# Optimization experiments

Hardware: AMD Instinct MI355X
Metric: run time of the kernel (lower is better)

## Reference

```python
import jax, jax.numpy as jnp
import numpy as np

SIGMA = 1.0
RADIUS = 4  # skimage.filters.gaussian: truncate=4.0 -> radius=int(4.0*1.0+0.5)=4 (9 taps)
NBINS = 256  # skimage.filters.threshold_otsu default


def _gauss_kernel(dtype):
    x = jnp.arange(-RADIUS, RADIUS + 1, dtype=dtype)
    k = jnp.exp(-0.5 * (x / SIGMA) ** 2)
    return k / k.sum()


def _blur(img):
    # img: [B, H, W]; separable Gaussian, 'nearest' (edge) boundary like scipy/skimage.
    k = _gauss_kernel(img.dtype)
    p = jnp.pad(img, ((0, 0), (RADIUS, RADIUS), (0, 0)), mode='edge')
    out = jax.lax.conv_general_dilated(p[:, None], k.reshape(1, 1, 2 * RADIUS + 1, 1),
                                       (1, 1), 'VALID')[:, 0]
    p = jnp.pad(out, ((0, 0), (0, 0), (RADIUS, RADIUS)), mode='edge')
    out = jax.lax.conv_general_dilated(p[:, None], k.reshape(1, 1, 1, 2 * RADIUS + 1),
                                       (1, 1), 'VALID')[:, 0]
    return out


def _otsu(img):
    # img: [H, W] -> scalar Otsu threshold (256-bin histogram over [min, max]).
    lo, hi = img.min(), img.max()
    width = (hi - lo) / NBINS
    idx = jnp.clip(jnp.floor((img - lo) / jnp.maximum(width, 1e-12)).astype(jnp.int32),
                   0, NBINS - 1)
    counts = jnp.zeros(NBINS, img.dtype).at[idx.ravel()].add(1.0)
    centers = lo + (jnp.arange(NBINS, dtype=img.dtype) + 0.5) * width
    w1 = jnp.cumsum(counts)                      # class-0 weight
    w2 = jnp.cumsum(counts[::-1])[::-1]          # class-1 weight
    cs = jnp.cumsum(counts * centers)
    rcs = jnp.cumsum((counts * centers)[::-1])[::-1]
    m1 = cs / jnp.maximum(w1, 1e-12)
    m2 = rcs / jnp.maximum(w2, 1e-12)
    var12 = w1[:-1] * w2[1:] * (m1[:-1] - m2[1:]) ** 2
    return centers[jnp.argmax(var12)]


def reference(x):
    # x: [B, 4, H, W]; channel 0 = thermal (normalized mean=std=0.5), last 3 = RGB.
    thermal = jnp.clip(x[:, 0] * 0.5 + 0.5, 0.0, 1.0)          # denormalize [B,H,W]
    blurred = _blur(thermal)
    t = jax.vmap(_otsu)(blurred)                               # [B]
    mask = jnp.where(blurred > t[:, None, None], 1.0, blurred)  # soft alpha mask
    rgb = x[:, -3:]                                            # [B,3,H,W]
    alpha = mask[:, None]                                      # [B,1,H,W]
    # skimage rgba2rgb with white background: clip(alpha*rgb + (1-alpha)*1)
    return jnp.clip(alpha * rgb + (1.0 - alpha), 0.0, 1.0)


def setup_inputs() -> dict:
    key = jax.random.key(0)
    x = jax.random.normal(key, (32, 4, 512, 512), dtype=jnp.float32)
    return {"x": x}
```

## Files before the change

### kernel.cpp

```cpp
#include <hip/hip_runtime.h>
#include <math.h>

#pragma clang fp contract(off)

struct GaussW { float w[9]; };

__global__ __launch_bounds__(256) void blur_kernel(const float* __restrict__ x,
                                                   float* __restrict__ blurred,
                                                   float* __restrict__ pmin,
                                                   float* __restrict__ pmax,
                                                   unsigned* __restrict__ hist, GaussW gw) {
    #pragma clang fp contract(off)
    __shared__ float s_in[72][72];
    __shared__ float s_vb[64][72];
    const int tid = threadIdx.x;
    const int b = blockIdx.z;
    const int r0 = blockIdx.y * 64, c0 = blockIdx.x * 64;
    if (blockIdx.x == 0 && blockIdx.y == 0) hist[b * 256 + tid] = 0u;
    const float* img0 = x + (size_t)b * 4 * 262144;

    for (int i = tid; i < 72 * 72; i += 256) {
        int r = i / 72, c = i - r * 72;
        int gr = min(max(r0 + r - 4, 0), 511);
        int gc = min(max(c0 + c - 4, 0), 511);
        float v = img0[gr * 512 + gc];
        s_in[r][c] = fminf(fmaxf(v * 0.5f + 0.5f, 0.0f), 1.0f);
    }
    __syncthreads();
    for (int i = tid; i < 1152; i += 256) {
        int sr = (i / 72) * 4, c = i % 72;
        float t0 = s_in[sr + 0][c], t1 = s_in[sr + 1][c], t2 = s_in[sr + 2][c];
        float t3 = s_in[sr + 3][c], t4 = s_in[sr + 4][c], t5 = s_in[sr + 5][c];
        float t6 = s_in[sr + 6][c], t7 = s_in[sr + 7][c], t8 = s_in[sr + 8][c];
        float t9 = s_in[sr + 9][c], t10 = s_in[sr + 10][c], t11 = s_in[sr + 11][c];
        {
            float q0 = t0 * gw.w[0], q1 = t1 * gw.w[1], q2 = t2 * gw.w[2], q3 = t3 * gw.w[3];
            float q4 = t4 * gw.w[4], q5 = t5 * gw.w[5], q6 = t6 * gw.w[6], q7 = t7 * gw.w[7];
            float acc = ((q0 + q1) + (q2 + q3)) + ((q4 + q5) + (q6 + q7));
            s_vb[sr + 0][c] = acc + t8 * gw.w[8];
        }
        {
            float q0 = t1 * gw.w[0], q1 = t2 * gw.w[1], q2 = t3 * gw.w[2], q3 = t4 * gw.w[3];
            float q4 = t5 * gw.w[4], q5 = t6 * gw.w[5], q6 = t7 * gw.w[6], q7 = t8 * gw.w[7];
            float acc = ((q0 + q1) + (q2 + q3)) + ((q4 + q5) + (q6 + q7));
            s_vb[sr + 1][c] = acc + t9 * gw.w[8];
        }
        {
            float q0 = t2 * gw.w[0], q1 = t3 * gw.w[1], q2 = t4 * gw.w[2], q3 = t5 * gw.w[3];
            float q4 = t6 * gw.w[4], q5 = t7 * gw.w[5], q6 = t8 * gw.w[6], q7 = t9 * gw.w[7];
            float acc = ((q0 + q1) + (q2 + q3)) + ((q4 + q5) + (q6 + q7));
            s_vb[sr + 2][c] = acc + t10 * gw.w[8];
        }
        {
            float q0 = t3 * gw.w[0], q1 = t4 * gw.w[1], q2 = t5 * gw.w[2], q3 = t6 * gw.w[3];
            float q4 = t7 * gw.w[4], q5 = t8 * gw.w[5], q6 = t9 * gw.w[6], q7 = t10 * gw.w[7];
            float acc = ((q0 + q1) + (q2 + q3)) + ((q4 + q5) + (q6 + q7));
            s_vb[sr + 3][c] = acc + t11 * gw.w[8];
        }
    }
    __syncthreads();
    float lmin = 1e30f, lmax = -1e30f;
    float* bimg = blurred + (size_t)b * 262144;
    for (int i = tid; i < 1024; i += 256) {
        int r = i >> 4, cc = (i & 15) * 4;
        float4 va = *(const float4*)&s_vb[r][cc];
        float4 vb = *(const float4*)&s_vb[r][cc + 4];
        float4 vc = *(const float4*)&s_vb[r][cc + 8];
        float t0 = va.x, t1 = va.y, t2 = va.z, t3 = va.w;
        float t4 = vb.x, t5 = vb.y, t6 = vb.z, t7 = vb.w;
        float t8 = vc.x, t9 = vc.y, t10 = vc.z, t11 = vc.w;
        float4 o;
        {
            float q0 = t0 * gw.w[0], q1 = t1 * gw.w[1], q2 = t2 * gw.w[2], q3 = t3 * gw.w[3];
            float q4 = t4 * gw.w[4], q5 = t5 * gw.w[5], q6 = t6 * gw.w[6], q7 = t7 * gw.w[7];
            float acc = ((q0 + q1) + (q2 + q3)) + ((q4 + q5) + (q6 + q7));
            o.x = acc + t8 * gw.w[8];
        }
        {
            float q0 = t1 * gw.w[0], q1 = t2 * gw.w[1], q2 = t3 * gw.w[2], q3 = t4 * gw.w[3];
            float q4 = t5 * gw.w[4], q5 = t6 * gw.w[5], q6 = t7 * gw.w[6], q7 = t8 * gw.w[7];
            float acc = ((q0 + q1) + (q2 + q3)) + ((q4 + q5) + (q6 + q7));
            o.y = acc + t9 * gw.w[8];
        }
        {
            float q0 = t2 * gw.w[0], q1 = t3 * gw.w[1], q2 = t4 * gw.w[2], q3 = t5 * gw.w[3];
            float q4 = t6 * gw.w[4], q5 = t7 * gw.w[5], q6 = t8 * gw.w[6], q7 = t9 * gw.w[7];
            float acc = ((q0 + q1) + (q2 + q3)) + ((q4 + q5) + (q6 + q7));
            o.z = acc + t10 * gw.w[8];
        }
        {
            float q0 = t3 * gw.w[0], q1 = t4 * gw.w[1], q2 = t5 * gw.w[2], q3 = t6 * gw.w[3];
            float q4 = t7 * gw.w[4], q5 = t8 * gw.w[5], q6 = t9 * gw.w[6], q7 = t10 * gw.w[7];
            float acc = ((q0 + q1) + (q2 + q3)) + ((q4 + q5) + (q6 + q7));
            o.w = acc + t11 * gw.w[8];
        }
        *(float4*)&bimg[(size_t)(r0 + r) * 512 + (c0 + cc)] = o;
        lmin = fminf(fminf(fminf(lmin, o.x), fminf(o.y, o.z)), o.w);
        lmax = fmaxf(fmaxf(fmaxf(lmax, o.x), fmaxf(o.y, o.z)), o.w);
    }
    for (int off = 32; off >= 1; off >>= 1) {
        lmin = fminf(lmin, __shfl_down(lmin, off));
        lmax = fmaxf(lmax, __shfl_down(lmax, off));
    }
    __shared__ float smin[4], smax[4];
    int wave = tid >> 6, lane = tid & 63;
    if (lane == 0) { smin[wave] = lmin; smax[wave] = lmax; }
    __syncthreads();
    if (tid == 0) {
        float mn = fminf(fminf(smin[0], smin[1]), fminf(smin[2], smin[3]));
        float mx = fmaxf(fmaxf(smax[0], smax[1]), fmaxf(smax[2], smax[3]));
        int bid = blockIdx.y * 8 + blockIdx.x;
        pmin[b * 64 + bid] = mn;
        pmax[b * 64 + bid] = mx;
    }
}

__global__ __launch_bounds__(256) void hist_kernel(const float* __restrict__ blurred,
                                                   const float* __restrict__ pmin,
                                                   const float* __restrict__ pmax,
                                                   unsigned* __restrict__ hist) {
    #pragma clang fp contract(off)
    const int b = blockIdx.y;
    __shared__ unsigned sh[2048];
    __shared__ float s_lo, s_hi;
    for (int i = threadIdx.x; i < 2048; i += 256) sh[i] = 0u;
    int wv = threadIdx.x >> 6, ln = threadIdx.x & 63;
    if (wv == 0) {
        float v = pmin[b * 64 + ln];
        for (int off = 32; off >= 1; off >>= 1) v = fminf(v, __shfl_down(v, off));
        if (ln == 0) s_lo = v;
    } else if (wv == 1) {
        float v = pmax[b * 64 + ln];
        for (int off = 32; off >= 1; off >>= 1) v = fmaxf(v, __shfl_down(v, off));
        if (ln == 0) s_hi = v;
    }
    __syncthreads();
    const float lo = s_lo, hi = s_hi;
    const float width = (hi - lo) * 0.00390625f;
    const float denom = fmaxf(width, 1e-12f);
    const int copy = threadIdx.x & 7;
    const float4* img = (const float4*)(blurred + (size_t)b * 262144);
    for (int i = blockIdx.x * 256 + threadIdx.x; i < 65536; i += gridDim.x * 256) {
        float4 v = img[i];
        int i0 = min(max((int)floorf((v.x - lo) / denom), 0), 255);
        int i1 = min(max((int)floorf((v.y - lo) / denom), 0), 255);
        int i2 = min(max((int)floorf((v.z - lo) / denom), 0), 255);
        int i3 = min(max((int)floorf((v.w - lo) / denom), 0), 255);
        atomicAdd(&sh[i0 * 8 + copy], 1u);
        atomicAdd(&sh[i1 * 8 + copy], 1u);
        atomicAdd(&sh[i2 * 8 + copy], 1u);
        atomicAdd(&sh[i3 * 8 + copy], 1u);
    }
    __syncthreads();
    unsigned cnt = 0;
    int base = threadIdx.x * 8;
#pragma unroll
    for (int k = 0; k < 8; ++k) cnt += sh[base + k];
    if (cnt) atomicAdd(&hist[b * 256 + threadIdx.x], cnt);
}

__global__ __launch_bounds__(256) void otsu_kernel(const unsigned* __restrict__ hist,
                                                   const float* __restrict__ pmin,
                                                   const float* __restrict__ pmax,
                                                   float* __restrict__ t) {
    #pragma clang fp contract(off)
    __shared__ float counts[256], centers[256], w1[256], w2[256], cs[256], rcs[256];
    __shared__ float s_lo, s_hi;
    const int b = blockIdx.x, tid = threadIdx.x;
    const int wv = tid >> 6, ln = tid & 63;
    if (wv == 0) {
        float v = pmin[b * 64 + ln];
        for (int off = 32; off >= 1; off >>= 1) v = fminf(v, __shfl_down(v, off));
        if (ln == 0) s_lo = v;
    } else if (wv == 1) {
        float v = pmax[b * 64 + ln];
        for (int off = 32; off >= 1; off >>= 1) v = fmaxf(v, __shfl_down(v, off));
        if (ln == 0) s_hi = v;
    }
    __syncthreads();
    const float lo = s_lo, hi = s_hi;
    const float width = (hi - lo) * 0.00390625f;
    counts[tid] = (float)hist[b * 256 + tid];
    centers[tid] = lo + ((float)tid + 0.5f) * width;
    __syncthreads();
    if (ln == 0) {
        if (wv == 0) {
            float a = 0.f;
            for (int i0 = 0; i0 < 256; i0 += 8) {
                float c0 = counts[i0+0], c1 = counts[i0+1], c2 = counts[i0+2], c3 = counts[i0+3];
                float c4 = counts[i0+4], c5 = counts[i0+5], c6 = counts[i0+6], c7 = counts[i0+7];
                a = a + c0; w1[i0+0] = a; a = a + c1; w1[i0+1] = a;
                a = a + c2; w1[i0+2] = a; a = a + c3; w1[i0+3] = a;
                a = a + c4; w1[i0+4] = a; a = a + c5; w1[i0+5] = a;
                a = a + c6; w1[i0+6] = a; a = a + c7; w1[i0+7] = a;
            }
        } else if (wv == 1) {
            float a = 0.f;
            for (int i0 = 255; i0 >= 7; i0 -= 8) {
                float c0 = counts[i0-0], c1 = counts[i0-1], c2 = counts[i0-2], c3 = counts[i0-3];
                float c4 = counts[i0-4], c5 = counts[i0-5], c6 = counts[i0-6], c7 = counts[i0-7];
                a = a + c0; w2[i0-0] = a; a = a + c1; w2[i0-1] = a;
                a = a + c2; w2[i0-2] = a; a = a + c3; w2[i0-3] = a;
                a = a + c4; w2[i0-4] = a; a = a + c5; w2[i0-5] = a;
                a = a + c6; w2[i0-6] = a; a = a + c7; w2[i0-7] = a;
            }
        } else if (wv == 2) {
            float a = 0.f;
            for (int i0 = 0; i0 < 256; i0 += 8) {
                float q0 = counts[i0+0] * centers[i0+0], q1 = counts[i0+1] * centers[i0+1];
                float q2 = counts[i0+2] * centers[i0+2], q3 = counts[i0+3] * centers[i0+3];
                float q4 = counts[i0+4] * centers[i0+4], q5 = counts[i0+5] * centers[i0+5];
                float q6 = counts[i0+6] * centers[i0+6], q7 = counts[i0+7] * centers[i0+7];
                a = a + q0; cs[i0+0] = a; a = a + q1; cs[i0+1] = a;
                a = a + q2; cs[i0+2] = a; a = a + q3; cs[i0+3] = a;
                a = a + q4; cs[i0+4] = a; a = a + q5; cs[i0+5] = a;
                a = a + q6; cs[i0+6] = a; a = a + q7; cs[i0+7] = a;
            }
        } else {
            float a = 0.f;
            for (int i0 = 255; i0 >= 7; i0 -= 8) {
                float q0 = counts[i0-0] * centers[i0-0], q1 = counts[i0-1] * centers[i0-1];
                float q2 = counts[i0-2] * centers[i0-2], q3 = counts[i0-3] * centers[i0-3];
                float q4 = counts[i0-4] * centers[i0-4], q5 = counts[i0-5] * centers[i0-5];
                float q6 = counts[i0-6] * centers[i0-6], q7 = counts[i0-7] * centers[i0-7];
                a = a + q0; rcs[i0-0] = a; a = a + q1; rcs[i0-1] = a;
                a = a + q2; rcs[i0-2] = a; a = a + q3; rcs[i0-3] = a;
                a = a + q4; rcs[i0-4] = a; a = a + q5; rcs[i0-5] = a;
                a = a + q6; rcs[i0-6] = a; a = a + q7; rcs[i0-7] = a;
            }
        }
    }
    __syncthreads();
    if (wv == 0) {
        float best = -1e30f; int bi = 0x7fffffff;
#pragma unroll
        for (int k = 0; k < 4; ++k) {
            int i = ln + 64 * k;
            if (i < 255) {
                float m1 = cs[i] / fmaxf(w1[i], 1e-12f);
                float m2 = rcs[i + 1] / fmaxf(w2[i + 1], 1e-12f);
                float d = m1 - m2;
                float v = (w1[i] * w2[i + 1]) * (d * d);
                if (v > best) { best = v; bi = i; }
            }
        }
        for (int off = 32; off >= 1; off >>= 1) {
            float ov = __shfl_down(best, off);
            int   oi = __shfl_down(bi, off);
            if (ov > best || (ov == best && oi < bi)) { best = ov; bi = oi; }
        }
        if (ln == 0) t[b] = centers[bi];
    }
}

__global__ __launch_bounds__(256) void final_kernel(const float* __restrict__ x,
                                                    const float* __restrict__ blurred,
                                                    const float* __restrict__ tarr,
                                                    float* __restrict__ out, int total4) {
    #pragma clang fp contract(off)
    int i = blockIdx.x * 256 + threadIdx.x;
    if (i >= total4) return;
    int b = i >> 16;
    int p = i & 65535;
    float tb = tarr[b];
    float4 bl = ((const float4*)(blurred + (size_t)b * 262144))[p];
    float4 m;
    m.x = (bl.x > tb) ? 1.0f : bl.x;
    m.y = (bl.y > tb) ? 1.0f : bl.y;
    m.z = (bl.z > tb) ? 1.0f : bl.z;
    m.w = (bl.w > tb) ? 1.0f : bl.w;
    const float4* xim = (const float4*)(x + (size_t)b * 4 * 262144);
    float4* oim = (float4*)(out + (size_t)b * 3 * 262144);
#pragma unroll
    for (int c = 0; c < 3; ++c) {
        float4 rgb = xim[(size_t)(c + 1) * 65536 + p];
        float4 o;
        o.x = fminf(fmaxf(m.x * rgb.x + (1.0f - m.x), 0.f), 1.f);
        o.y = fminf(fmaxf(m.y * rgb.y + (1.0f - m.y), 0.f), 1.f);
        o.z = fminf(fmaxf(m.z * rgb.z + (1.0f - m.z), 0.f), 1.f);
        o.w = fminf(fmaxf(m.w * rgb.w + (1.0f - m.w), 0.f), 1.f);
        oim[(size_t)c * 65536 + p] = o;
    }
}

extern "C" void kernel_launch(void* const* d_in, const int* in_sizes, int n_in,
                              void* d_out, int out_size, void* d_ws, size_t ws_size,
                              hipStream_t stream) {
    const float* x = (const float*)d_in[0];
    float* out = (float*)d_out;
    const int nimg = in_sizes[0] / (4 * 262144);

    float* blurred = (float*)d_ws;
    unsigned* hist = (unsigned*)(blurred + (size_t)nimg * 262144);
    float* pmin = (float*)(hist + (size_t)nimg * 256);
    float* pmax = pmin + (size_t)nimg * 64;
    float* t = pmax + (size_t)nimg * 64;

    GaussW gw;
    float kk[9];
    for (int i = 0; i < 9; ++i) {
        double d = (double)(i - 4);
        kk[i] = (float)exp(-0.5 * d * d);
    }
    float s = ((kk[0] + kk[1]) + (kk[2] + kk[3])) + ((kk[4] + kk[5]) + (kk[6] + kk[7]));
    s = s + kk[8];
    for (int i = 0; i < 9; ++i) gw.w[i] = kk[i] / s;

    dim3 bgrid(8, 8, nimg);
    blur_kernel<<<bgrid, 256, 0, stream>>>(x, blurred, pmin, pmax, hist, gw);
    dim3 hgrid(16, nimg);
    hist_kernel<<<hgrid, 256, 0, stream>>>(blurred, pmin, pmax, hist);
    otsu_kernel<<<nimg, 256, 0, stream>>>(hist, pmin, pmax, t);
    int total4 = nimg * 65536;
    final_kernel<<<(total4 + 255) / 256, 256, 0, stream>>>(x, blurred, t, out, total4);
}
```

Before: 254.0 us.

## Fuse blur, histogram, Otsu and compositing into one cooperative persistent kernel

Replaces the four separate kernel launches with a single cooperative kernel on a fixed grid of 1024 blocks that loops over blur tiles, histogram chunks and final pixels, separated by grid-wide syncs. A per-image counter lets the last histogram block of each image compute the Otsu threshold inline, so the separate Otsu launch goes away. The aim is to remove launch gaps and tail effects between stages. In exchange it adds grid-sync overhead and caps occupancy at the cooperative grid size, with shared memory unioned across phases.

```diff
diff --git a/kernel.cpp b/kernel.cpp
--- a/kernel.cpp
+++ b/kernel.cpp
@@ -1,285 +1,290 @@
 #include <hip/hip_runtime.h>
+#include <hip/hip_cooperative_groups.h>
 #include <math.h>
 
 #pragma clang fp contract(off)
 
+namespace cg = cooperative_groups;
+
 struct GaussW { float w[9]; };
 
-__global__ __launch_bounds__(256) void blur_kernel(const float* __restrict__ x,
-                                                   float* __restrict__ blurred,
-                                                   float* __restrict__ pmin,
-                                                   float* __restrict__ pmax,
-                                                   unsigned* __restrict__ hist, GaussW gw) {
+__global__ __launch_bounds__(256, 4) void mono_kernel(const float* __restrict__ x,
+                                                      float* __restrict__ blurred,
+                                                      float* __restrict__ pmin,
+                                                      float* __restrict__ pmax,
+                                                      unsigned* __restrict__ hist,
+                                                      unsigned* __restrict__ cnt,
+                                                      float* __restrict__ t,
+                                                      float* __restrict__ out,
+                                                      GaussW gw, int nimg) {
     #pragma clang fp contract(off)
-    __shared__ float s_in[72][72];
-    __shared__ float s_vb[64][72];
+    __shared__ union {
+        struct { float s_in[72][72]; float s_vb[64][72]; } b;
+        struct { unsigned sh[2048]; } h;
+        struct { float counts[256], centers[256], w1[256], w2[256], cs[256], rcs[256]; } o;
+    } u;
+    __shared__ float s_lo, s_hi;
+    __shared__ float smin[4], smax[4];
+    __shared__ int s_last;
+
     const int tid = threadIdx.x;
-    const int b = blockIdx.z;
-    const int r0 = blockIdx.y * 64, c0 = blockIdx.x * 64;
-    if (blockIdx.x == 0 && blockIdx.y == 0) hist[b * 256 + tid] = 0u;
-    const float* img0 = x + (size_t)b * 4 * 262144;
-
-    for (int i = tid; i < 72 * 72; i += 256) {
-        int r = i / 72, c = i - r * 72;
-        int gr = min(max(r0 + r - 4, 0), 511);
-        int gc = min(max(c0 + c - 4, 0), 511);
-        float v = img0[gr * 512 + gc];
-        s_in[r][c] = fminf(fmaxf(v * 0.5f + 0.5f, 0.0f), 1.0f);
-    }
-    __syncthreads();
-    for (int i = tid; i < 1152; i += 256) {
-        int sr = (i / 72) * 4, c = i % 72;
-        float t0 = s_in[sr + 0][c], t1 = s_in[sr + 1][c], t2 = s_in[sr + 2][c];
-        float t3 = s_in[sr + 3][c], t4 = s_in[sr + 4][c], t5 = s_in[sr + 5][c];
-        float t6 = s_in[sr + 6][c], t7 = s_in[sr + 7][c], t8 = s_in[sr + 8][c];
-        float t9 = s_in[sr + 9][c], t10 = s_in[sr + 10][c], t11 = s_in[sr + 11][c];
+    const int wv = tid >> 6, ln = tid & 63;
+    cg::grid_group grid = cg::this_grid();
+
+    if (blockIdx.x < (unsigned)nimg) {
+        hist[blockIdx.x * 256 + tid] = 0u;
+        if (tid == 0) cnt[blockIdx.x] = 0u;
+    }
+
+    const int ntiles = nimg * 64;
+    for (int tile = blockIdx.x; tile < ntiles; tile += gridDim.x) {
+        const int b = tile >> 6, ty = (tile >> 3) & 7, tx = tile & 7;
+        const int r0 = ty * 64, c0 = tx * 64;
+        const float* img0 = x + (size_t)b * 4 * 262144;
+        __syncthreads();
+        for (int i = tid; i < 72 * 72; i += 256) {
+            int r = i / 72, c = i - r * 72;
+            int gr = min(max(r0 + r - 4, 0), 511);
+            int gc = min(max(c0 + c - 4, 0), 511);
+            float v = img0[gr * 512 + gc];
+            u.b.s_in[r][c] = fminf(fmaxf(v * 0.5f + 0.5f, 0.0f), 1.0f);
+        }
+        __syncthreads();
+        for (int i = tid; i < 1152; i += 256) {
+            int sr = (i / 72) * 4, c = i % 72;
+            float t0 = u.b.s_in[sr + 0][c], t1 = u.b.s_in[sr + 1][c], t2 = u.b.s_in[sr + 2][c];
+            float t3 = u.b.s_in[sr + 3][c], t4 = u.b.s_in[sr + 4][c], t5 = u.b.s_in[sr + 5][c];
+            float t6 = u.b.s_in[sr + 6][c], t7 = u.b.s_in[sr + 7][c], t8 = u.b.s_in[sr + 8][c];
+            float t9 = u.b.s_in[sr + 9][c], t10 = u.b.s_in[sr + 10][c], t11 = u.b.s_in[sr + 11][c];
+            {
+                float q0 = t0 * gw.w[0], q1 = t1 * gw.w[1], q2 = t2 * gw.w[2], q3 = t3 * gw.w[3];
+                float q4 = t4 * gw.w[4], q5 = t5 * gw.w[5], q6 = t6 * gw.w[6], q7 = t7 * gw.w[7];
+                float acc = ((q0 + q1) + (q2 + q3)) + ((q4 + q5) + (q6 + q7));
+                u.b.s_vb[sr + 0][c] = acc + t8 * gw.w[8];
+            }
+            {
+                float q0 = t1 * gw.w[0], q1 = t2 * gw.w[1], q2 = t3 * gw.w[2], q3 = t4 * gw.w[3];
+                float q4 = t5 * gw.w[4], q5 = t6 * gw.w[5], q6 = t7 * gw.w[6], q7 = t8 * gw.w[7];
+                float acc = ((q0 + q1) + (q2 + q3)) + ((q4 + q5) + (q6 + q7));
+                u.b.s_vb[sr + 1][c] = acc + t9 * gw.w[8];
+            }
+            {
+                float q0 = t2 * gw.w[0], q1 = t3 * gw.w[1], q2 = t4 * gw.w[2], q3 = t5 * gw.w[3];
+                float q4 = t6 * gw.w[4], q5 = t7 * gw.w[5], q6 = t8 * gw.w[6], q7 = t9 * gw.w[7];
+                float acc = ((q0 + q1) + (q2 + q3)) + ((q4 + q5) + (q6 + q7));
+                u.b.s_vb[sr + 2][c] = acc + t10 * gw.w[8];
+            }
+            {
+                float q0 = t3 * gw.w[0], q1 = t4 * gw.w[1], q2 = t5 * gw.w[2], q3 = t6 * gw.w[3];
+                float q4 = t7 * gw.w[4], q5 = t8 * gw.w[5], q6 = t9 * gw.w[6], q7 = t10 * gw.w[7];
+                float acc = ((q0 + q1) + (q2 + q3)) + ((q4 + q5) + (q6 + q7));
+                u.b.s_vb[sr + 3][c] = acc + t11 * gw.w[8];
+            }
+        }
+        __syncthreads();
+        float lmin = 1e30f, lmax = -1e30f;
+        float* bimg = blurred + (size_t)b * 262144;
+        for (int i = tid; i < 1024; i += 256) {
+            int r = i >> 4, cc = (i & 15) * 4;
+            float4 va = *(const float4*)&u.b.s_vb[r][cc];
+            float4 vb = *(const float4*)&u.b.s_vb[r][cc + 4];
+            float4 vc = *(const float4*)&u.b.s_vb[r][cc + 8];
+            float t0 = va.x, t1 = va.y, t2 = va.z, t3 = va.w;
+            float t4 = vb.x, t5 = vb.y, t6 = vb.z, t7 = vb.w;
+            float t8 = vc.x, t9 = vc.y, t10 = vc.z, t11 = vc.w;
+            float4 o;
+            {
+                float q0 = t0 * gw.w[0], q1 = t1 * gw.w[1], q2 = t2 * gw.w[2], q3 = t3 * gw.w[3];
+                float q4 = t4 * gw.w[4], q5 = t5 * gw.w[5], q6 = t6 * gw.w[6], q7 = t7 * gw.w[7];
+                float acc = ((q0 + q1) + (q2 + q3)) + ((q4 + q5) + (q6 + q7));
+                o.x = acc + t8 * gw.w[8];
+            }
+            {
+                float q0 = t1 * gw.w[0], q1 = t2 * gw.w[1], q2 = t3 * gw.w[2], q3 = t4 * gw.w[3];
+                float q4 = t5 * gw.w[4], q5 = t6 * gw.w[5], q6 = t7 * gw.w[6], q7 = t8 * gw.w[7];
+                float acc = ((q0 + q1) + (q2 + q3)) + ((q4 + q5) + (q6 + q7));
+                o.y = acc + t9 * gw.w[8];
+            }
+            {
+                float q0 = t2 * gw.w[0], q1 = t3 * gw.w[1], q2 = t4 * gw.w[2], q3 = t5 * gw.w[3];
+                float q4 = t6 * gw.w[4], q5 = t7 * gw.w[5], q6 = t8 * gw.w[6], q7 = t9 * gw.w[7];
+                float acc = ((q0 + q1) + (q2 + q3)) + ((q4 + q5) + (q6 + q7));
+                o.z = acc + t10 * gw.w[8];
+            }
+            {
+                float q0 = t3 * gw.w[0], q1 = t4 * gw.w[1], q2 = t5 * gw.w[2], q3 = t6 * gw.w[3];
+                float q4 = t7 * gw.w[4], q5 = t8 * gw.w[5], q6 = t9 * gw.w[6], q7 = t10 * gw.w[7];
+                float acc = ((q0 + q1) + (q2 + q3)) + ((q4 + q5) + (q6 + q7));
+                o.w = acc + t11 * gw.w[8];
+            }
+            *(float4*)&bimg[(size_t)(r0 + r) * 512 + (c0 + cc)] = o;
+            lmin = fminf(fminf(fminf(lmin, o.x), fminf(o.y, o.z)), o.w);
+            lmax = fmaxf(fmaxf(fmaxf(lmax, o.x), fmaxf(o.y, o.z)), o.w);
+        }
+        for (int off = 32; off >= 1; off >>= 1) {
+            lmin = fminf(lmin, __shfl_down(lmin, off));
+            lmax = fmaxf(lmax, __shfl_down(lmax, off));
+        }
+        if (ln == 0) { smin[wv] = lmin; smax[wv] = lmax; }
+        __syncthreads();
+        if (tid == 0) {
+            float mn = fminf(fminf(smin[0], smin[1]), fminf(smin[2], smin[3]));
+            float mx = fmaxf(fmaxf(smax[0], smax[1]), fmaxf(smax[2], smax[3]));
+            int bid = ty * 8 + tx;
+            pmin[b * 64 + bid] = mn;
+            pmax[b * 64 + bid] = mx;
+        }
+    }
+
+    grid.sync();
+
+    const int nunits = nimg * 32;
+    for (int unit = blockIdx.x; unit < nunits; unit += gridDim.x) {
+        const int b = unit >> 5, chunk = unit & 31;
+        __syncthreads();
+        for (int i = tid; i < 2048; i += 256) u.h.sh[i] = 0u;
+        if (wv == 0) {
+            float v = pmin[b * 64 + ln];
+            for (int off = 32; off >= 1; off >>= 1) v = fminf(v, __shfl_down(v, off));
+            if (ln == 0) s_lo = v;
+        } else if (wv == 1) {
+            float v = pmax[b * 64 + ln];
+            for (int off = 32; off >= 1; off >>= 1) v = fmaxf(v, __shfl_down(v, off));
+            if (ln == 0) s_hi = v;
+        }
+        __syncthreads();
+        const float lo = s_lo, hi = s_hi;
+        const float width = (hi - lo) * 0.00390625f;
+        const float denom = fmaxf(width, 1e-12f);
+        const int copy = tid & 7;
+        const float4* img = (const float4*)(blurred + (size_t)b * 262144);
+        for (int i = chunk * 2048 + tid; i < (chunk + 1) * 2048; i += 256) {
+            float4 v = img[i];
+            int i0 = min(max((int)floorf((v.x - lo) / denom), 0), 255);
+            int i1 = min(max((int)floorf((v.y - lo) / denom), 0), 255);
+            int i2 = min(max((int)floorf((v.z - lo) / denom), 0), 255);
+            int i3 = min(max((int)floorf((v.w - lo) / denom), 0), 255);
+            atomicAdd(&u.h.sh[i0 * 8 + copy], 1u);
+            atomicAdd(&u.h.sh[i1 * 8 + copy], 1u);
+            atomicAdd(&u.h.sh[i2 * 8 + copy], 1u);
+            atomicAdd(&u.h.sh[i3 * 8 + copy], 1u);
+        }
+        __syncthreads();
+        unsigned c8 = 0;
         {
-            float q0 = t0 * gw.w[0], q1 = t1 * gw.w[1], q2 = t2 * gw.w[2], q3 = t3 * gw.w[3];
-            float q4 = t4 * gw.w[4], q5 = t5 * gw.w[5], q6 = t6 * gw.w[6], q7 = t7 * gw.w[7];
-            float acc = ((q0 + q1) + (q2 + q3)) + ((q4 + q5) + (q6 + q7));
-            s_vb[sr + 0][c] = acc + t8 * gw.w[8];
-        }
-        {
-            float q0 = t1 * gw.w[0], q1 = t2 * gw.w[1], q2 = t3 * gw.w[2], q3 = t4 * gw.w[3];
-            float q4 = t5 * gw.w[4], q5 = t6 * gw.w[5], q6 = t7 * gw.w[6], q7 = t8 * gw.w[7];
-            float acc = ((q0 + q1) + (q2 + q3)) + ((q4 + q5) + (q6 + q7));
-            s_vb[sr + 1][c] = acc + t9 * gw.w[8];
-        }
-        {
-            float q0 = t2 * gw.w[0], q1 = t3 * gw.w[1], q2 = t4 * gw.w[2], q3 = t5 * gw.w[3];
-            float q4 = t6 * gw.w[4], q5 = t7 * gw.w[5], q6 = t8 * gw.w[6], q7 = t9 * gw.w[7];
-            float acc = ((q0 + q1) + (q2 + q3)) + ((q4 + q5) + (q6 + q7));
-            s_vb[sr + 2][c] = acc + t10 * gw.w[8];
-        }
-        {
-            float q0 = t3 * gw.w[0], q1 = t4 * gw.w[1], q2 = t5 * gw.w[2], q3 = t6 * gw.w[3];
-            float q4 = t7 * gw.w[4], q5 = t8 * gw.w[5], q6 = t9 * gw.w[6], q7 = t10 * gw.w[7];
-            float acc = ((q0 + q1) + (q2 + q3)) + ((q4 + q5) + (q6 + q7));
-            s_vb[sr + 3][c] = acc + t11 * gw.w[8];
-        }
-    }
-    __syncthreads();
-    float lmin = 1e30f, lmax = -1e30f;
-    float* bimg = blurred + (size_t)b * 262144;
-    for (int i = tid; i < 1024; i += 256) {
-        int r = i >> 4, cc = (i & 15) * 4;
-        float4 va = *(const float4*)&s_vb[r][cc];
-        float4 vb = *(const float4*)&s_vb[r][cc + 4];
-        float4 vc = *(const float4*)&s_vb[r][cc + 8];
-        float t0 = va.x, t1 = va.y, t2 = va.z, t3 = va.w;
-        float t4 = vb.x, t5 = vb.y, t6 = vb.z, t7 = vb.w;
-        float t8 = vc.x, t9 = vc.y, t10 = vc.z, t11 = vc.w;
-        float4 o;
-        {
-            float q0 = t0 * gw.w[0], q1 = t1 * gw.w[1], q2 = t2 * gw.w[2], q3 = t3 * gw.w[3];
-            float q4 = t4 * gw.w[4], q5 = t5 * gw.w[5], q6 = t6 * gw.w[6], q7 = t7 * gw.w[7];
-            float acc = ((q0 + q1) + (q2 + q3)) + ((q4 + q5) + (q6 + q7));
-            o.x = acc + t8 * gw.w[8];
-        }
-        {
-            float q0 = t1 * gw.w[0], q1 = t2 * gw.w[1], q2 = t3 * gw.w[2], q3 = t4 * gw.w[3];
-            float q4 = t5 * gw.w[4], q5 = t6 * gw.w[5], q6 = t7 * gw.w[6], q7 = t8 * gw.w[7];
-            float acc = ((q0 + q1) + (q2 + q3)) + ((q4 + q5) + (q6 + q7));
-            o.y = acc + t9 * gw.w[8];
-        }
-        {
-            float q0 = t2 * gw.w[0], q1 = t3 * gw.w[1], q2 = t4 * gw.w[2], q3 = t5 * gw.w[3];
-            float q4 = t6 * gw.w[4], q5 = t7 * gw.w[5], q6 = t8 * gw.w[6], q7 = t9 * gw.w[7];
-            float acc = ((q0 + q1) + (q2 + q3)) + ((q4 + q5) + (q6 + q7));
-            o.z = acc + t10 * gw.w[8];
-        }
-        {
-            float q0 = t3 * gw.w[0], q1 = t4 * gw.w[1], q2 = t5 * gw.w[2], q3 = t6 * gw.w[3];
-            float q4 = t7 * gw.w[4], q5 = t8 * gw.w[5], q6 = t9 * gw.w[6], q7 = t10 * gw.w[7];
-            float acc = ((q0 + q1) + (q2 + q3)) + ((q4 + q5) + (q6 + q7));
-            o.w = acc + t11 * gw.w[8];
-        }
-        *(float4*)&bimg[(size_t)(r0 + r) * 512 + (c0 + cc)] = o;
-        lmin = fminf(fminf(fminf(lmin, o.x), fminf(o.y, o.z)), o.w);
-        lmax = fmaxf(fmaxf(fmaxf(lmax, o.x), fmaxf(o.y, o.z)), o.w);
-    }
-    for (int off = 32; off >= 1; off >>= 1) {
-        lmin = fminf(lmin, __shfl_down(lmin, off));
-        lmax = fmaxf(lmax, __shfl_down(lmax, off));
-    }
-    __shared__ float smin[4], smax[4];
-    int wave = tid >> 6, lane = tid & 63;
-    if (lane == 0) { smin[wave] = lmin; smax[wave] = lmax; }
-    __syncthreads();
-    if (tid == 0) {
-        float mn = fminf(fminf(smin[0], smin[1]), fminf(smin[2], smin[3]));
-        float mx = fmaxf(fmaxf(smax[0], smax[1]), fmaxf(smax[2], smax[3]));
-        int bid = blockIdx.y * 8 + blockIdx.x;
-        pmin[b * 64 + bid] = mn;
-        pmax[b * 64 + bid] = mx;
-    }
-}
-
-__global__ __launch_bounds__(256) void hist_kernel(const float* __restrict__ blurred,
-                                                   const float* __restrict__ pmin,
-                                                   const float* __restrict__ pmax,
-                                                   unsigned* __restrict__ hist) {
-    #pragma clang fp contract(off)
-    const int b = blockIdx.y;
-    __shared__ unsigned sh[2048];
-    __shared__ float s_lo, s_hi;
-    for (int i = threadIdx.x; i < 2048; i += 256) sh[i] = 0u;
-    int wv = threadIdx.x >> 6, ln = threadIdx.x & 63;
-    if (wv == 0) {
-        float v = pmin[b * 64 + ln];
-        for (int off = 32; off >= 1; off >>= 1) v = fminf(v, __shfl_down(v, off));
-        if (ln == 0) s_lo = v;
-    } else if (wv == 1) {
-        float v = pmax[b * 64 + ln];
-        for (int off = 32; off >= 1; off >>= 1) v = fmaxf(v, __shfl_down(v, off));
-        if (ln == 0) s_hi = v;
-    }
-    __syncthreads();
-    const float lo = s_lo, hi = s_hi;
-    const float width = (hi - lo) * 0.00390625f;
-    const float denom = fmaxf(width, 1e-12f);
-    const int copy = threadIdx.x & 7;
-    const float4* img = (const float4*)(blurred + (size_t)b * 262144);
-    for (int i = blockIdx.x * 256 + threadIdx.x; i < 65536; i += gridDim.x * 256) {
-        float4 v = img[i];
-        int i0 = min(max((int)floorf((v.x - lo) / denom), 0), 255);
-        int i1 = min(max((int)floorf((v.y - lo) / denom), 0), 255);
-        int i2 = min(max((int)floorf((v.z - lo) / denom), 0), 255);
-        int i3 = min(max((int)floorf((v.w - lo) / denom), 0), 255);
-        atomicAdd(&sh[i0 * 8 + copy], 1u);
-        atomicAdd(&sh[i1 * 8 + copy], 1u);
-        atomicAdd(&sh[i2 * 8 + copy], 1u);
-        atomicAdd(&sh[i3 * 8 + copy], 1u);
-    }
-    __syncthreads();
-    unsigned cnt = 0;
-    int base = threadIdx.x * 8;
+            int base = tid * 8;
 #pragma unroll
-    for (int k = 0; k < 8; ++k) cnt += sh[base + k];
-    if (cnt) atomicAdd(&hist[b * 256 + threadIdx.x], cnt);
-}
-
-__global__ __launch_bounds__(256) void otsu_kernel(const unsigned* __restrict__ hist,
-                                                   const float* __restrict__ pmin,
-                                                   const float* __restrict__ pmax,
-                                                   float* __restrict__ t) {
-    #pragma clang fp contract(off)
-    __shared__ float counts[256], centers[256], w1[256], w2[256], cs[256], rcs[256];
-    __shared__ float s_lo, s_hi;
-    const int b = blockIdx.x, tid = threadIdx.x;
-    const int wv = tid >> 6, ln = tid & 63;
-    if (wv == 0) {
-        float v = pmin[b * 64 + ln];
-        for (int off = 32; off >= 1; off >>= 1) v = fminf(v, __shfl_down(v, off));
-        if (ln == 0) s_lo = v;
-    } else if (wv == 1) {
-        float v = pmax[b * 64 + ln];
-        for (int off = 32; off >= 1; off >>= 1) v = fmaxf(v, __shfl_down(v, off));
-        if (ln == 0) s_hi = v;
-    }
-    __syncthreads();
-    const float lo = s_lo, hi = s_hi;
-    const float width = (hi - lo) * 0.00390625f;
-    counts[tid] = (float)hist[b * 256 + tid];
-    centers[tid] = lo + ((float)tid + 0.5f) * width;
-    __syncthreads();
-    if (ln == 0) {
-        if (wv == 0) {
-            float a = 0.f;
-            for (int i0 = 0; i0 < 256; i0 += 8) {
-                float c0 = counts[i0+0], c1 = counts[i0+1], c2 = counts[i0+2], c3 = counts[i0+3];
-                float c4 = counts[i0+4], c5 = counts[i0+5], c6 = counts[i0+6], c7 = counts[i0+7];
-                a = a + c0; w1[i0+0] = a; a = a + c1; w1[i0+1] = a;
-                a = a + c2; w1[i0+2] = a; a = a + c3; w1[i0+3] = a;
-                a = a + c4; w1[i0+4] = a; a = a + c5; w1[i0+5] = a;
-                a = a + c6; w1[i0+6] = a; a = a + c7; w1[i0+7] = a;
-            }
-        } else if (wv == 1) {
-            float a = 0.f;
-            for (int i0 = 255; i0 >= 7; i0 -= 8) {
-                float c0 = counts[i0-0], c1 = counts[i0-1], c2 = counts[i0-2], c3 = counts[i0-3];
-                float c4 = counts[i0-4], c5 = counts[i0-5], c6 = counts[i0-6], c7 = counts[i0-7];
-                a = a + c0; w2[i0-0] = a; a = a + c1; w2[i0-1] = a;
-                a = a + c2; w2[i0-2] = a; a = a + c3; w2[i0-3] = a;
-                a = a + c4; w2[i0-4] = a; a = a + c5; w2[i0-5] = a;
-                a = a + c6; w2[i0-6] = a; a = a + c7; w2[i0-7] = a;
-            }
-        } else if (wv == 2) {
-            float a = 0.f;
-            for (int i0 = 0; i0 < 256; i0 += 8) {
-                float q0 = counts[i0+0] * centers[i0+0], q1 = counts[i0+1] * centers[i0+1];
-                float q2 = counts[i0+2] * centers[i0+2], q3 = counts[i0+3] * centers[i0+3];
-                float q4 = counts[i0+4] * centers[i0+4], q5 = counts[i0+5] * centers[i0+5];
-                float q6 = counts[i0+6] * centers[i0+6], q7 = counts[i0+7] * centers[i0+7];
-                a = a + q0; cs[i0+0] = a; a = a + q1; cs[i0+1] = a;
-                a = a + q2; cs[i0+2] = a; a = a + q3; cs[i0+3] = a;
-                a = a + q4; cs[i0+4] = a; a = a + q5; cs[i0+5] = a;
-                a = a + q6; cs[i0+6] = a; a = a + q7; cs[i0+7] = a;
-            }
-        } else {
-            float a = 0.f;
-            for (int i0 = 255; i0 >= 7; i0 -= 8) {
-                float q0 = counts[i0-0] * centers[i0-0], q1 = counts[i0-1] * centers[i0-1];
-                float q2 = counts[i0-2] * centers[i0-2], q3 = counts[i0-3] * centers[i0-3];
-                float q4 = counts[i0-4] * centers[i0-4], q5 = counts[i0-5] * centers[i0-5];
-                float q6 = counts[i0-6] * centers[i0-6], q7 = counts[i0-7] * centers[i0-7];
-                a = a + q0; rcs[i0-0] = a; a = a + q1; rcs[i0-1] = a;
-                a = a + q2; rcs[i0-2] = a; a = a + q3; rcs[i0-3] = a;
-                a = a + q4; rcs[i0-4] = a; a = a + q5; rcs[i0-5] = a;
-                a = a + q6; rcs[i0-6] = a; a = a + q7; rcs[i0-7] = a;
-            }
-        }
-    }
-    __syncthreads();
-    if (wv == 0) {
-        float best = -1e30f; int bi = 0x7fffffff;
+            for (int k = 0; k < 8; ++k) c8 += u.h.sh[base + k];
+        }
+        if (c8) atomicAdd(&hist[b * 256 + tid], c8);
+        __threadfence();
+        __syncthreads();
+        if (tid == 0) {
+            unsigned v = atomicAdd(&cnt[b], 1u);
+            s_last = (v == 31u);
+        }
+        __syncthreads();
+        if (s_last) {
+            __threadfence();
+            u.o.counts[tid] = (float)hist[b * 256 + tid];
+            u.o.centers[tid] = lo + ((float)tid + 0.5f) * width;
+            __syncthreads();
+            if (ln == 0) {
+                if (wv == 0) {
+                    float a = 0.f;
+                    for (int i0 = 0; i0 < 256; i0 += 8) {
+                        float c0 = u.o.counts[i0+0], c1 = u.o.counts[i0+1], c2 = u.o.counts[i0+2], c3 = u.o.counts[i0+3];
+                        float c4 = u.o.counts[i0+4], c5 = u.o.counts[i0+5], c6 = u.o.counts[i0+6], c7 = u.o.counts[i0+7];
+                        a = a + c0; u.o.w1[i0+0] = a; a = a + c1; u.o.w1[i0+1] = a;
+                        a = a + c2; u.o.w1[i0+2] = a; a = a + c3; u.o.w1[i0+3] = a;
+                        a = a + c4; u.o.w1[i0+4] = a; a = a + c5; u.o.w1[i0+5] = a;
+                        a = a + c6; u.o.w1[i0+6] = a; a = a + c7; u.o.w1[i0+7] = a;
+                    }
+                } else if (wv == 1) {
+                    float a = 0.f;
+                    for (int i0 = 255; i0 >= 7; i0 -= 8) {
+                        float c0 = u.o.counts[i0-0], c1 = u.o.counts[i0-1], c2 = u.o.counts[i0-2], c3 = u.o.counts[i0-3];
+                        float c4 = u.o.counts[i0-4], c5 = u.o.counts[i0-5], c6 = u.o.counts[i0-6], c7 = u.o.counts[i0-7];
+                        a = a + c0; u.o.w2[i0-0] = a; a = a + c1; u.o.w2[i0-1] = a;
+                        a = a + c2; u.o.w2[i0-2] = a; a = a + c3; u.o.w2[i0-3] = a;
+                        a = a + c4; u.o.w2[i0-4] = a; a = a + c5; u.o.w2[i0-5] = a;
+                        a = a + c6; u.o.w2[i0-6] = a; a = a + c7; u.o.w2[i0-7] = a;
+                    }
+                } else if (wv == 2) {
+                    float a = 0.f;
+                    for (int i0 = 0; i0 < 256; i0 += 8) {
+                        float q0 = u.o.counts[i0+0] * u.o.centers[i0+0], q1 = u.o.counts[i0+1] * u.o.centers[i0+1];
+                        float q2 = u.o.counts[i0+2] * u.o.centers[i0+2], q3 = u.o.counts[i0+3] * u.o.centers[i0+3];
+                        float q4 = u.o.counts[i0+4] * u.o.centers[i0+4], q5 = u.o.counts[i0+5] * u.o.centers[i0+5];
+                        float q6 = u.o.counts[i0+6] * u.o.centers[i0+6], q7 = u.o.counts[i0+7] * u.o.centers[i0+7];
+                        a = a + q0; u.o.cs[i0+0] = a; a = a + q1; u.o.cs[i0+1] = a;
+                        a = a + q2; u.o.cs[i0+2] = a; a = a + q3; u.o.cs[i0+3] = a;
+                        a = a + q4; u.o.cs[i0+4] = a; a = a + q5; u.o.cs[i0+5] = a;
+                        a = a + q6; u.o.cs[i0+6] = a; a = a + q7; u.o.cs[i0+7] = a;
+                    }
+                } else {
+                    float a = 0.f;
+                    for (int i0 = 255; i0 >= 7; i0 -= 8) {
+                        float q0 = u.o.counts[i0-0] * u.o.centers[i0-0], q1 = u.o.counts[i0-1] * u.o.centers[i0-1];
+                        float q2 = u.o.counts[i0-2] * u.o.centers[i0-2], q3 = u.o.counts[i0-3] * u.o.centers[i0-3];
+                        float q4 = u.o.counts[i0-4] * u.o.centers[i0-4], q5 = u.o.counts[i0-5] * u.o.centers[i0-5];
+                        float q6 = u.o.counts[i0-6] * u.o.centers[i0-6], q7 = u.o.counts[i0-7] * u.o.centers[i0-7];
+                        a = a + q0; u.o.rcs[i0-0] = a; a = a + q1; u.o.rcs[i0-1] = a;
+                        a = a + q2; u.o.rcs[i0-2] = a; a = a + q3; u.o.rcs[i0-3] = a;
+                        a = a + q4; u.o.rcs[i0-4] = a; a = a + q5; u.o.rcs[i0-5] = a;
+                        a = a + q6; u.o.rcs[i0-6] = a; a = a + q7; u.o.rcs[i0-7] = a;
+                    }
+                }
+            }
+            __syncthreads();
+            if (wv == 0) {
+                float best = -1e30f; int bi = 0x7fffffff;
 #pragma unroll
-        for (int k = 0; k < 4; ++k) {
-            int i = ln + 64 * k;
-            if (i < 255) {
-                float m1 = cs[i] / fmaxf(w1[i], 1e-12f);
-                float m2 = rcs[i + 1] / fmaxf(w2[i + 1], 1e-12f);
-                float d = m1 - m2;
-                float v = (w1[i] * w2[i + 1]) * (d * d);
-                if (v > best) { best = v; bi = i; }
-            }
-        }
-        for (int off = 32; off >= 1; off >>= 1) {
-            float ov = __shfl_down(best, off);
-            int   oi = __shfl_down(bi, off);
-            if (ov > best || (ov == best && oi < bi)) { best = ov; bi = oi; }
-        }
-        if (ln == 0) t[b] = centers[bi];
-    }
-}
-
-__global__ __launch_bounds__(256) void final_kernel(const float* __restrict__ x,
-                                                    const float* __restrict__ blurred,
-                                                    const float* __restrict__ tarr,
-                                                    float* __restrict__ out, int total4) {
-    #pragma clang fp contract(off)
-    int i = blockIdx.x * 256 + threadIdx.x;
-    if (i >= total4) return;
-    int b = i >> 16;
-    int p = i & 65535;
-    float tb = tarr[b];
-    float4 bl = ((const float4*)(blurred + (size_t)b * 262144))[p];
-    float4 m;
-    m.x = (bl.x > tb) ? 1.0f : bl.x;
-    m.y = (bl.y > tb) ? 1.0f : bl.y;
-    m.z = (bl.z > tb) ? 1.0f : bl.z;
-    m.w = (bl.w > tb) ? 1.0f : bl.w;
-    const float4* xim = (const float4*)(x + (size_t)b * 4 * 262144);
-    float4* oim = (float4*)(out + (size_t)b * 3 * 262144);
+                for (int k = 0; k < 4; ++k) {
+                    int i = ln + 64 * k;
+                    if (i < 255) {
+                        float m1 = u.o.cs[i] / fmaxf(u.o.w1[i], 1e-12f);
+                        float m2 = u.o.rcs[i + 1] / fmaxf(u.o.w2[i + 1], 1e-12f);
+                        float d = m1 - m2;
+                        float v = (u.o.w1[i] * u.o.w2[i + 1]) * (d * d);
+                        if (v > best) { best = v; bi = i; }
+                    }
+                }
+                for (int off = 32; off >= 1; off >>= 1) {
+                    float ov = __shfl_down(best, off);
+                    int   oi = __shfl_down(bi, off);
+                    if (ov > best || (ov == best && oi < bi)) { best = ov; bi = oi; }
+                }
+                if (ln == 0) t[b] = u.o.centers[bi];
+            }
+        }
+    }
+
+    grid.sync();
+
+    const int total4 = nimg * 65536;
+    for (int i = blockIdx.x * 256 + tid; i < total4; i += gridDim.x * 256) {
+        int b = i >> 16;
+        int p = i & 65535;
+        float tb = t[b];
+        float4 bl = ((const float4*)(blurred + (size_t)b * 262144))[p];
+        float4 m;
+        m.x = (bl.x > tb) ? 1.0f : bl.x;
+        m.y = (bl.y > tb) ? 1.0f : bl.y;
+        m.z = (bl.z > tb) ? 1.0f : bl.z;
+        m.w = (bl.w > tb) ? 1.0f : bl.w;
+        const float4* xim = (const float4*)(x + (size_t)b * 4 * 262144);
+        float4* oim = (float4*)(out + (size_t)b * 3 * 262144);
 #pragma unroll
-    for (int c = 0; c < 3; ++c) {
-        float4 rgb = xim[(size_t)(c + 1) * 65536 + p];
-        float4 o;
-        o.x = fminf(fmaxf(m.x * rgb.x + (1.0f - m.x), 0.f), 1.f);
-        o.y = fminf(fmaxf(m.y * rgb.y + (1.0f - m.y), 0.f), 1.f);
-        o.z = fminf(fmaxf(m.z * rgb.z + (1.0f - m.z), 0.f), 1.f);
-        o.w = fminf(fmaxf(m.w * rgb.w + (1.0f - m.w), 0.f), 1.f);
-        oim[(size_t)c * 65536 + p] = o;
+        for (int c = 0; c < 3; ++c) {
+            float4 rgb = xim[(size_t)(c + 1) * 65536 + p];
+            float4 o;
+            o.x = fminf(fmaxf(m.x * rgb.x + (1.0f - m.x), 0.f), 1.f);
+            o.y = fminf(fmaxf(m.y * rgb.y + (1.0f - m.y), 0.f), 1.f);
+            o.z = fminf(fmaxf(m.z * rgb.z + (1.0f - m.z), 0.f), 1.f);
+            o.w = fminf(fmaxf(m.w * rgb.w + (1.0f - m.w), 0.f), 1.f);
+            oim[(size_t)c * 65536 + p] = o;
+        }
     }
 }
 
@@ -288,11 +293,12 @@
                               hipStream_t stream) {
     const float* x = (const float*)d_in[0];
     float* out = (float*)d_out;
-    const int nimg = in_sizes[0] / (4 * 262144);
+    int nimg = in_sizes[0] / (4 * 262144);
 
     float* blurred = (float*)d_ws;
     unsigned* hist = (unsigned*)(blurred + (size_t)nimg * 262144);
-    float* pmin = (float*)(hist + (size_t)nimg * 256);
+    unsigned* cnt = hist + (size_t)nimg * 256;
+    float* pmin = (float*)(cnt + nimg);
     float* pmax = pmin + (size_t)nimg * 64;
     float* t = pmax + (size_t)nimg * 64;
 
@@ -306,11 +312,8 @@
     s = s + kk[8];
     for (int i = 0; i < 9; ++i) gw.w[i] = kk[i] / s;
 
-    dim3 bgrid(8, 8, nimg);
-    blur_kernel<<<bgrid, 256, 0, stream>>>(x, blurred, pmin, pmax, hist, gw);
-    dim3 hgrid(16, nimg);
-    hist_kernel<<<hgrid, 256, 0, stream>>>(blurred, pmin, pmax, hist);
-    otsu_kernel<<<nimg, 256, 0, stream>>>(hist, pmin, pmax, t);
-    int total4 = nimg * 65536;
-    final_kernel<<<(total4 + 255) / 256, 256, 0, stream>>>(x, blurred, t, out, total4);
+    void* args[] = { (void*)&x, (void*)&blurred, (void*)&pmin, (void*)&pmax,
+                     (void*)&hist, (void*)&cnt, (void*)&t, (void*)&out,
+                     (void*)&gw, (void*)&nimg };
+    hipLaunchCooperativeKernel((void*)mono_kernel, dim3(1024), dim3(256), args, 0, stream);
 }
```

After: 563.4 us. +121.8%, slower.
